# Performance work log

Measured on AMD Instinct MI355X. Metric: run time of the kernel, lower is better.

Reference implementation:

```python
import jax, jax.numpy as jnp
import numpy as np

T_V = 0.1
T_Q = 0.1
NEG_VIDEO_IOU = 0.5
POS_VIDEO_TOPK = 1
MARGIN = 0.0
EPS = 1e-12


def _normalize(x):
    # F.normalize(dim=-1) with eps clamp
    n = jnp.linalg.norm(x, axis=-1, keepdims=True)
    return x / jnp.maximum(n, EPS)


def _log_cross_entropy(pos_score, all_score, neg_mask, t, m):
    pos_exp = jnp.exp((pos_score - m) / t)
    neg_exp_sum = jnp.sum(jnp.exp(all_score / t) * neg_mask, axis=-1)
    loss = -((pos_score - m) / t - jnp.log(pos_exp + neg_exp_sum))
    return jnp.mean(loss)


def setup_inputs() -> dict:
    B, C, N, S = 32, 256, 64, 64
    key = jax.random.key(0)
    k1, k2, k3 = jax.random.split(key, 3)
    video_feats = jax.random.normal(k1, (B, C, N, N), dtype=jnp.float32)
    sents_feats = jax.random.normal(k2, (S, C), dtype=jnp.float32)
    iou2ds = jax.random.uniform(k3, (S, N, N), dtype=jnp.float32)
    mask2d = jnp.triu(jnp.ones((N, N), dtype=bool))  # P = N*(N+1)/2 = 2080
    num_targets = jnp.full((B,), S // B, dtype=jnp.int32)  # sums to S
    return {"video_feats": video_feats, "sents_feats": sents_feats,
            "num_targets": num_targets, "iou2ds": iou2ds, "mask2d": mask2d}


def reference(video_feats, sents_feats, num_targets, iou2ds, mask2d):
    B, C, N, _ = video_feats.shape
    S = sents_feats.shape[0]
    K = POS_VIDEO_TOPK
    # mask2d / num_targets are structural constants -> resolve on host
    flat_idx = np.nonzero(np.asarray(mask2d).reshape(-1))[0]   # [P]
    P = flat_idx.shape[0]
    scatter_idx = np.repeat(np.arange(B), np.asarray(num_targets))  # [S]

    # masked_select of valid proposals
    vf = video_feats.reshape(B, C, N * N)[:, :, flat_idx]      # [B,C,P]
    vf = jnp.transpose(vf, (0, 2, 1))                          # [B,P,C]
    iou = iou2ds.reshape(S, N * N)[:, flat_idx]                # [S,P]

    vf = _normalize(vf)
    sf = _normalize(sents_feats)                               # [S,C]

    # top-k proposals per sentence
    topk_idx = jax.lax.top_k(iou, K)[1]                        # [S,K]
    sv = vf[scatter_idx]                                       # [S,P,C]
    topk_video = jnp.take_along_axis(sv, topk_idx[:, :, None], axis=1)  # [S,K,C]

    # inter-video loss
    inter_video_pos = jnp.einsum('skc,sc->sk', topk_video, sf)          # [S,K]
    inter_video_all = jnp.einsum('skc,tc->skt', topk_video, sf)         # [S,K,S]
    inter_video_neg_mask = (~jnp.eye(S, dtype=bool))[:, None, :]        # [S,1,S]
    loss_inter_video = _log_cross_entropy(
        inter_video_pos, inter_video_all, inter_video_neg_mask, T_V, MARGIN)

    # inter-query loss
    inter_query_all = jnp.einsum('sc,bpc->sbp', sf, vf).reshape(S, 1, B * P)
    same_video = jnp.asarray(scatter_idx)[:, None] == jnp.arange(B)[None, :]  # [S,B]
    pos_mask = same_video[:, :, None] & (iou > NEG_VIDEO_IOU)[:, None, :]     # [S,B,P]
    inter_query_neg_mask = (~pos_mask).reshape(S, 1, B * P)
    loss_inter_query = _log_cross_entropy(
        inter_video_pos, inter_query_all, inter_query_neg_mask, T_Q, MARGIN)

    return (loss_inter_video, loss_inter_query)
```

## Files before the change

### kernel.cpp

```cpp
#include <hip/hip_runtime.h>
#include <hip/hip_bf16.h>
#include <math.h>

constexpr int B_ = 32;
constexpr int C_ = 256;
constexpr int N_ = 64;
constexpr int S_ = 64;
constexpr int NPIX = N_ * N_;
constexpr int QB = B_ * N_;

#define T_V_INV 10.0f
#define T_Q_INV 10.0f
#define NEG_IOU 0.5f

typedef __attribute__((ext_vector_type(8))) short short8;
typedef __attribute__((ext_vector_type(4))) float f32x4;

static __device__ __forceinline__ unsigned short f2bf(float x) {
  __hip_bfloat16 h = __float2bfloat16(x);
  unsigned short u;
  __builtin_memcpy(&u, &h, sizeof(u));
  return u;
}

__global__ void k_prep(const float* __restrict__ sents,
                       float* __restrict__ sf_t,
                       unsigned short* __restrict__ sf_frag) {
  int s = blockIdx.x, c = threadIdx.x;
  __shared__ float wsum[4];
  float v = sents[s * C_ + c];
  float ss = v * v;
  #pragma unroll
  for (int o = 32; o; o >>= 1) ss += __shfl_xor(ss, o);
  if ((c & 63) == 0) wsum[c >> 6] = ss;
  __syncthreads();
  float tot = wsum[0] + wsum[1] + wsum[2] + wsum[3];
  float rn = 1.0f / fmaxf(sqrtf(tot), 1e-12f);
  float o = v * rn;
  sf_t[c * S_ + s] = o;
  int ks = c >> 5, q = (c >> 3) & 3, j = c & 7;
  int mt = s >> 4, m = s & 15;
  int lane = q * 16 + m;
  sf_frag[((ks * 4 + mt) * 64 + lane) * 8 + j] = f2bf(o);
}

__global__ void k_scatter(const int* __restrict__ nt, int* __restrict__ scatter) {
  int s = threadIdx.x;
  int cum = 0, res = 0;
  for (int b = 0; b < B_; b++) {
    int nb = nt[b];
    if (s >= cum && s < cum + nb) res = b;
    cum += nb;
  }
  scatter[s] = res;
}

__global__ void k_topk(const float* __restrict__ iou, int* __restrict__ top_pix) {
  int s = blockIdx.x, tid = threadIdx.x;
  __shared__ float bval[256];
  __shared__ int bidx[256];
  float bv = -1.0f;
  int bi = 0x7fffffff;
  for (int pix = tid; pix < NPIX; pix += 256) {
    int r = pix >> 6, c0 = pix & 63;
    if (c0 >= r) {
      float v = iou[s * NPIX + pix];
      if (v > bv) { bv = v; bi = pix; }
    }
  }
  bval[tid] = bv; bidx[tid] = bi;
  __syncthreads();
  for (int st = 128; st; st >>= 1) {
    if (tid < st) {
      float ov = bval[tid + st]; int oi = bidx[tid + st];
      if (ov > bval[tid] || (ov == bval[tid] && oi < bidx[tid])) {
        bval[tid] = ov; bidx[tid] = oi;
      }
    }
    __syncthreads();
  }
  if (tid == 0) top_pix[s] = bidx[0];
}

__global__ void k_video(const float* __restrict__ V,
                        const float* __restrict__ sf_t,
                        const int* __restrict__ scatter,
                        const int* __restrict__ top_pix,
                        float* __restrict__ pos_score,
                        float* __restrict__ loss_vid) {
  int s = blockIdx.x, t = threadIdx.x;
  __shared__ float vh[C_];
  int b = scatter[s];
  int pix = top_pix[s];
  const float* vp = V + ((size_t)b * C_) * NPIX + pix;
  float vloc[4];
  float ss = 0.0f;
  #pragma unroll
  for (int k = 0; k < 4; k++) {
    vloc[k] = vp[(size_t)(t + 64 * k) * NPIX];
    ss = fmaf(vloc[k], vloc[k], ss);
  }
  #pragma unroll
  for (int o = 32; o; o >>= 1) ss += __shfl_xor(ss, o);
  float rn = 1.0f / fmaxf(sqrtf(ss), 1e-12f);
  #pragma unroll
  for (int k = 0; k < 4; k++) vh[t + 64 * k] = vloc[k] * rn;
  __syncthreads();
  float dot = 0.0f;
  #pragma unroll 8
  for (int c = 0; c < C_; c++) dot = fmaf(vh[c], sf_t[c * S_ + t], dot);
  if (t == s) pos_score[s] = dot;
  float pos = __shfl(dot, s);
  float e = (t == s) ? 0.0f : __expf(dot * T_V_INV);
  #pragma unroll
  for (int o = 32; o; o >>= 1) e += __shfl_xor(e, o);
  if (t == 0) {
    float pp = pos * T_V_INV;
    loss_vid[s] = -(pp - logf(__expf(pp) + e));
  }
}

__global__ __launch_bounds__(256) void k_query(
    const float* __restrict__ V, const float* __restrict__ iou,
    const short8* __restrict__ Afrag, const int* __restrict__ scatter,
    float* __restrict__ partials) {
  __shared__ int ssc[S_];
  __shared__ float part[4][S_];
  int tid = threadIdx.x;
  if (tid < S_) ssc[tid] = scatter[tid];
  __syncthreads();

  int b = blockIdx.x >> 6, r = blockIdx.x & 63;
  int w = tid >> 6, lane = tid & 63;
  int n = lane & 15, q = lane >> 4;
  int col = w * 16 + n;
  int pix = r * 64 + col;
  bool active = (col >= r);

  const float* vb = V + (size_t)b * C_ * NPIX + pix;
  f32x4 acc[4] = {f32x4{0,0,0,0}, f32x4{0,0,0,0}, f32x4{0,0,0,0}, f32x4{0,0,0,0}};
  float ssq = 0.0f;

  for (int ks = 0; ks < 8; ks++) {
    short8 bfrag;
    #pragma unroll
    for (int j = 0; j < 8; j++) {
      int c = ks * 32 + q * 8 + j;
      float v = active ? vb[(size_t)c * NPIX] : 0.0f;
      ssq = fmaf(v, v, ssq);
      bfrag[j] = (short)f2bf(v);
    }
    #pragma unroll
    for (int mt = 0; mt < 4; mt++) {
      short8 a = Afrag[(ks * 4 + mt) * 64 + lane];
      acc[mt] = __builtin_amdgcn_mfma_f32_16x16x32_bf16(a, bfrag, acc[mt], 0, 0, 0);
    }
  }

  ssq += __shfl_xor(ssq, 16);
  ssq += __shfl_xor(ssq, 32);
  float rs = T_Q_INV / fmaxf(sqrtf(ssq), 1e-12f);

  #pragma unroll
  for (int mt = 0; mt < 4; mt++) {
    #pragma unroll
    for (int rr = 0; rr < 4; rr++) {
      int s = mt * 16 + q * 4 + rr;
      float e = active ? __expf(acc[mt][rr] * rs) : 0.0f;
      if (active && ssc[s] == b) {
        if (iou[s * NPIX + pix] > NEG_IOU) e = 0.0f;
      }
      e += __shfl_xor(e, 1);
      e += __shfl_xor(e, 2);
      e += __shfl_xor(e, 4);
      e += __shfl_xor(e, 8);
      if (n == 0) part[w][s] = e;
    }
  }
  __syncthreads();
  if (tid < S_) {
    partials[(size_t)blockIdx.x * S_ + tid] =
        part[0][tid] + part[1][tid] + part[2][tid] + part[3][tid];
  }
}

__global__ void k_loss(const float* __restrict__ partials,
                       const float* __restrict__ pos_score,
                       float* __restrict__ loss_q) {
  int s = blockIdx.x, tid = threadIdx.x;
  __shared__ float wsum[4];
  float acc = 0.0f;
  for (int blk = tid; blk < QB; blk += 256) acc += partials[(size_t)blk * S_ + s];
  #pragma unroll
  for (int o = 32; o; o >>= 1) acc += __shfl_xor(acc, o);
  if ((tid & 63) == 0) wsum[tid >> 6] = acc;
  __syncthreads();
  if (tid == 0) {
    float neg = wsum[0] + wsum[1] + wsum[2] + wsum[3];
    float p = pos_score[s] * T_Q_INV;
    loss_q[s] = -(p - logf(__expf(p) + neg));
  }
}

__global__ void k_final(const float* __restrict__ loss_vid,
                        const float* __restrict__ loss_q,
                        float* __restrict__ out) {
  int tid = threadIdx.x;
  float lv = loss_vid[tid];
  float lq = loss_q[tid];
  #pragma unroll
  for (int o = 32; o; o >>= 1) {
    lv += __shfl_xor(lv, o);
    lq += __shfl_xor(lq, o);
  }
  if (tid == 0) {
    out[0] = lv / (float)S_;
    out[1] = lq / (float)S_;
  }
}

extern "C" void kernel_launch(void* const* d_in, const int* in_sizes, int n_in,
                              void* d_out, int out_size, void* d_ws, size_t ws_size,
                              hipStream_t stream) {
  const float* V     = (const float*)d_in[0];
  const float* sents = (const float*)d_in[1];
  const int*   nt    = (const int*)d_in[2];
  const float* iou   = (const float*)d_in[3];

  float* ws = (float*)d_ws;
  float*          sf_t    = ws;
  unsigned short* sf_frag = (unsigned short*)(ws + 16384);
  int*   scatter   = (int*)(ws + 16384 + 8192);
  int*   top_pix   = scatter + S_;
  float* pos_score = (float*)(top_pix + S_);
  float* loss_vid  = pos_score + S_;
  float* loss_q    = loss_vid + S_;
  float* partials  = loss_q + S_;

  k_prep   <<<S_, 256, 0, stream>>>(sents, sf_t, sf_frag);
  k_scatter<<<1, 64, 0, stream>>>(nt, scatter);
  k_topk   <<<S_, 256, 0, stream>>>(iou, top_pix);
  k_video  <<<S_, 64, 0, stream>>>(V, sf_t, scatter, top_pix, pos_score, loss_vid);
  k_query  <<<QB, 256, 0, stream>>>(V, iou, (const short8*)sf_frag, scatter, partials);
  k_loss   <<<S_, 256, 0, stream>>>(partials, pos_score, loss_q);
  k_final  <<<1, 64, 0, stream>>>(loss_vid, loss_q, (float*)d_out);
}
```

Baseline: 238.2 us.

## Fuse seven kernel launches into three: setup, main, and tail reduction

Merges sentence normalization, scatter computation and top-k into one setup kernel. The video-loss computation now runs as extra blocks appended to the query MFMA grid. The partial-sum reduction and final averaging are folded into a single 1024-thread tail kernel. This removes launch overhead and serialization between small kernels, but the tail reduction is now done by a single block instead of 64 blocks.

```diff
diff --git a/kernel.cpp b/kernel.cpp
--- a/kernel.cpp
+++ b/kernel.cpp
@@ -23,199 +23,198 @@
   return u;
 }
 
-__global__ void k_prep(const float* __restrict__ sents,
-                       float* __restrict__ sf_t,
-                       unsigned short* __restrict__ sf_frag) {
-  int s = blockIdx.x, c = threadIdx.x;
+__global__ __launch_bounds__(256) void k_setup(
+    const float* __restrict__ sents, const float* __restrict__ iou,
+    const int* __restrict__ nt,
+    float* __restrict__ sf_t, unsigned short* __restrict__ sf_frag,
+    int* __restrict__ scatter, int* __restrict__ top_pix) {
+  int bid = blockIdx.x, tid = threadIdx.x;
   __shared__ float wsum[4];
-  float v = sents[s * C_ + c];
-  float ss = v * v;
-  #pragma unroll
-  for (int o = 32; o; o >>= 1) ss += __shfl_xor(ss, o);
-  if ((c & 63) == 0) wsum[c >> 6] = ss;
-  __syncthreads();
-  float tot = wsum[0] + wsum[1] + wsum[2] + wsum[3];
-  float rn = 1.0f / fmaxf(sqrtf(tot), 1e-12f);
-  float o = v * rn;
-  sf_t[c * S_ + s] = o;
-  int ks = c >> 5, q = (c >> 3) & 3, j = c & 7;
-  int mt = s >> 4, m = s & 15;
-  int lane = q * 16 + m;
-  sf_frag[((ks * 4 + mt) * 64 + lane) * 8 + j] = f2bf(o);
-}
-
-__global__ void k_scatter(const int* __restrict__ nt, int* __restrict__ scatter) {
-  int s = threadIdx.x;
-  int cum = 0, res = 0;
-  for (int b = 0; b < B_; b++) {
-    int nb = nt[b];
-    if (s >= cum && s < cum + nb) res = b;
-    cum += nb;
-  }
-  scatter[s] = res;
-}
-
-__global__ void k_topk(const float* __restrict__ iou, int* __restrict__ top_pix) {
-  int s = blockIdx.x, tid = threadIdx.x;
   __shared__ float bval[256];
   __shared__ int bidx[256];
-  float bv = -1.0f;
-  int bi = 0x7fffffff;
-  for (int pix = tid; pix < NPIX; pix += 256) {
-    int r = pix >> 6, c0 = pix & 63;
-    if (c0 >= r) {
-      float v = iou[s * NPIX + pix];
-      if (v > bv) { bv = v; bi = pix; }
+
+  if (bid < S_) {
+    int s = bid, c = tid;
+    float v = sents[s * C_ + c];
+    float ss = v * v;
+    #pragma unroll
+    for (int o = 32; o; o >>= 1) ss += __shfl_xor(ss, o);
+    if ((c & 63) == 0) wsum[c >> 6] = ss;
+    __syncthreads();
+    float tot = wsum[0] + wsum[1] + wsum[2] + wsum[3];
+    float rn = 1.0f / fmaxf(sqrtf(tot), 1e-12f);
+    float o = v * rn;
+    sf_t[c * S_ + s] = o;
+    int ks = c >> 5, q = (c >> 3) & 3, j = c & 7;
+    int mt = s >> 4, m = s & 15;
+    sf_frag[((ks * 4 + mt) * 64 + (q * 16 + m)) * 8 + j] = f2bf(o);
+
+    float bv = -1.0f;
+    int bi = 0x7fffffff;
+    for (int pix = tid; pix < NPIX; pix += 256) {
+      int r = pix >> 6, c0 = pix & 63;
+      if (c0 >= r) {
+        float x = iou[s * NPIX + pix];
+        if (x > bv) { bv = x; bi = pix; }
+      }
+    }
+    bval[tid] = bv; bidx[tid] = bi;
+    __syncthreads();
+    for (int st = 128; st; st >>= 1) {
+      if (tid < st) {
+        float ov = bval[tid + st]; int oi = bidx[tid + st];
+        if (ov > bval[tid] || (ov == bval[tid] && oi < bidx[tid])) {
+          bval[tid] = ov; bidx[tid] = oi;
+        }
+      }
+      __syncthreads();
+    }
+    if (tid == 0) top_pix[s] = bidx[0];
+  } else {
+    if (tid < S_) {
+      int cum = 0, res = 0;
+      for (int b = 0; b < B_; b++) {
+        int nb = nt[b];
+        if (tid >= cum && tid < cum + nb) res = b;
+        cum += nb;
+      }
+      scatter[tid] = res;
     }
   }
-  bval[tid] = bv; bidx[tid] = bi;
-  __syncthreads();
-  for (int st = 128; st; st >>= 1) {
-    if (tid < st) {
-      float ov = bval[tid + st]; int oi = bidx[tid + st];
-      if (ov > bval[tid] || (ov == bval[tid] && oi < bidx[tid])) {
-        bval[tid] = ov; bidx[tid] = oi;
-      }
-    }
-    __syncthreads();
-  }
-  if (tid == 0) top_pix[s] = bidx[0];
-}
-
-__global__ void k_video(const float* __restrict__ V,
-                        const float* __restrict__ sf_t,
-                        const int* __restrict__ scatter,
-                        const int* __restrict__ top_pix,
-                        float* __restrict__ pos_score,
-                        float* __restrict__ loss_vid) {
-  int s = blockIdx.x, t = threadIdx.x;
-  __shared__ float vh[C_];
-  int b = scatter[s];
-  int pix = top_pix[s];
-  const float* vp = V + ((size_t)b * C_) * NPIX + pix;
-  float vloc[4];
-  float ss = 0.0f;
-  #pragma unroll
-  for (int k = 0; k < 4; k++) {
-    vloc[k] = vp[(size_t)(t + 64 * k) * NPIX];
-    ss = fmaf(vloc[k], vloc[k], ss);
-  }
-  #pragma unroll
-  for (int o = 32; o; o >>= 1) ss += __shfl_xor(ss, o);
-  float rn = 1.0f / fmaxf(sqrtf(ss), 1e-12f);
-  #pragma unroll
-  for (int k = 0; k < 4; k++) vh[t + 64 * k] = vloc[k] * rn;
-  __syncthreads();
-  float dot = 0.0f;
-  #pragma unroll 8
-  for (int c = 0; c < C_; c++) dot = fmaf(vh[c], sf_t[c * S_ + t], dot);
-  if (t == s) pos_score[s] = dot;
-  float pos = __shfl(dot, s);
-  float e = (t == s) ? 0.0f : __expf(dot * T_V_INV);
-  #pragma unroll
-  for (int o = 32; o; o >>= 1) e += __shfl_xor(e, o);
-  if (t == 0) {
-    float pp = pos * T_V_INV;
-    loss_vid[s] = -(pp - logf(__expf(pp) + e));
-  }
-}
-
-__global__ __launch_bounds__(256) void k_query(
+}
+
+__global__ __launch_bounds__(256) void k_main(
     const float* __restrict__ V, const float* __restrict__ iou,
-    const short8* __restrict__ Afrag, const int* __restrict__ scatter,
-    float* __restrict__ partials) {
+    const short8* __restrict__ Afrag, const float* __restrict__ sf_t,
+    const int* __restrict__ scatter, const int* __restrict__ top_pix,
+    float* __restrict__ partials, float* __restrict__ pos_score,
+    float* __restrict__ loss_vid) {
   __shared__ int ssc[S_];
   __shared__ float part[4][S_];
+  __shared__ float vh[C_];
+  __shared__ float red[4];
+  __shared__ float pdm[4][S_];
+
   int tid = threadIdx.x;
-  if (tid < S_) ssc[tid] = scatter[tid];
-  __syncthreads();
-
-  int b = blockIdx.x >> 6, r = blockIdx.x & 63;
-  int w = tid >> 6, lane = tid & 63;
-  int n = lane & 15, q = lane >> 4;
-  int col = w * 16 + n;
-  int pix = r * 64 + col;
-  bool active = (col >= r);
-
-  const float* vb = V + (size_t)b * C_ * NPIX + pix;
-  f32x4 acc[4] = {f32x4{0,0,0,0}, f32x4{0,0,0,0}, f32x4{0,0,0,0}, f32x4{0,0,0,0}};
-  float ssq = 0.0f;
-
-  for (int ks = 0; ks < 8; ks++) {
-    short8 bfrag;
-    #pragma unroll
-    for (int j = 0; j < 8; j++) {
-      int c = ks * 32 + q * 8 + j;
-      float v = active ? vb[(size_t)c * NPIX] : 0.0f;
-      ssq = fmaf(v, v, ssq);
-      bfrag[j] = (short)f2bf(v);
-    }
+
+  if (blockIdx.x < QB) {
+    if (tid < S_) ssc[tid] = scatter[tid];
+    __syncthreads();
+
+    int b = blockIdx.x >> 6, r = blockIdx.x & 63;
+    int w = tid >> 6, lane = tid & 63;
+    int n = lane & 15, q = lane >> 4;
+    int col = w * 16 + n;
+    int pix = r * 64 + col;
+    bool active = (col >= r);
+
+    const float* vb = V + (size_t)b * C_ * NPIX + pix;
+    f32x4 acc[4] = {f32x4{0,0,0,0}, f32x4{0,0,0,0}, f32x4{0,0,0,0}, f32x4{0,0,0,0}};
+    float ssq = 0.0f;
+
+    for (int ks = 0; ks < 8; ks++) {
+      short8 bfrag;
+      #pragma unroll
+      for (int j = 0; j < 8; j++) {
+        int c = ks * 32 + q * 8 + j;
+        float v = active ? vb[(size_t)c * NPIX] : 0.0f;
+        ssq = fmaf(v, v, ssq);
+        bfrag[j] = (short)f2bf(v);
+      }
+      #pragma unroll
+      for (int mt = 0; mt < 4; mt++) {
+        short8 a = Afrag[(ks * 4 + mt) * 64 + lane];
+        acc[mt] = __builtin_amdgcn_mfma_f32_16x16x32_bf16(a, bfrag, acc[mt], 0, 0, 0);
+      }
+    }
+
+    ssq += __shfl_xor(ssq, 16);
+    ssq += __shfl_xor(ssq, 32);
+    float rs = T_Q_INV / fmaxf(sqrtf(ssq), 1e-12f);
+
     #pragma unroll
     for (int mt = 0; mt < 4; mt++) {
-      short8 a = Afrag[(ks * 4 + mt) * 64 + lane];
-      acc[mt] = __builtin_amdgcn_mfma_f32_16x16x32_bf16(a, bfrag, acc[mt], 0, 0, 0);
+      #pragma unroll
+      for (int rr = 0; rr < 4; rr++) {
+        int s = mt * 16 + q * 4 + rr;
+        float e = active ? __expf(acc[mt][rr] * rs) : 0.0f;
+        if (active && ssc[s] == b) {
+          if (iou[s * NPIX + pix] > NEG_IOU) e = 0.0f;
+        }
+        e += __shfl_xor(e, 1);
+        e += __shfl_xor(e, 2);
+        e += __shfl_xor(e, 4);
+        e += __shfl_xor(e, 8);
+        if (n == 0) part[w][s] = e;
+      }
+    }
+    __syncthreads();
+    if (tid < S_) {
+      partials[(size_t)blockIdx.x * S_ + tid] =
+          part[0][tid] + part[1][tid] + part[2][tid] + part[3][tid];
+    }
+  } else {
+    int s = blockIdx.x - QB;
+    int b = scatter[s];
+    int pix = top_pix[s];
+    float v = V[((size_t)b * C_ + tid) * NPIX + pix];
+    float ss = v * v;
+    #pragma unroll
+    for (int o = 32; o; o >>= 1) ss += __shfl_xor(ss, o);
+    if ((tid & 63) == 0) red[tid >> 6] = ss;
+    __syncthreads();
+    float tot = red[0] + red[1] + red[2] + red[3];
+    float rn = 1.0f / fmaxf(sqrtf(tot), 1e-12f);
+    vh[tid] = v * rn;
+    __syncthreads();
+    int so = tid & 63, chunk = tid >> 6;
+    float pd = 0.0f;
+    #pragma unroll 8
+    for (int c = chunk * 64; c < chunk * 64 + 64; c++)
+      pd = fmaf(vh[c], sf_t[c * S_ + so], pd);
+    pdm[chunk][so] = pd;
+    __syncthreads();
+    if (tid < S_) {
+      float dot = pdm[0][tid] + pdm[1][tid] + pdm[2][tid] + pdm[3][tid];
+      if (tid == s) pos_score[s] = dot;
+      float pos = __shfl(dot, s);
+      float e = (tid == s) ? 0.0f : __expf(dot * T_V_INV);
+      #pragma unroll
+      for (int o = 32; o; o >>= 1) e += __shfl_xor(e, o);
+      if (tid == 0) {
+        float pp = pos * T_V_INV;
+        loss_vid[s] = -(pp - logf(__expf(pp) + e));
+      }
     }
   }
-
-  ssq += __shfl_xor(ssq, 16);
-  ssq += __shfl_xor(ssq, 32);
-  float rs = T_Q_INV / fmaxf(sqrtf(ssq), 1e-12f);
-
-  #pragma unroll
-  for (int mt = 0; mt < 4; mt++) {
-    #pragma unroll
-    for (int rr = 0; rr < 4; rr++) {
-      int s = mt * 16 + q * 4 + rr;
-      float e = active ? __expf(acc[mt][rr] * rs) : 0.0f;
-      if (active && ssc[s] == b) {
-        if (iou[s * NPIX + pix] > NEG_IOU) e = 0.0f;
-      }
-      e += __shfl_xor(e, 1);
-      e += __shfl_xor(e, 2);
-      e += __shfl_xor(e, 4);
-      e += __shfl_xor(e, 8);
-      if (n == 0) part[w][s] = e;
-    }
-  }
+}
+
+__global__ __launch_bounds__(1024) void k_tail(
+    const float* __restrict__ partials, const float* __restrict__ pos_score,
+    const float* __restrict__ loss_vid, float* __restrict__ out) {
+  int tid = threadIdx.x;
+  int s = tid & 63, g = tid >> 6;
+  __shared__ float m[16][S_];
+  float acc = 0.0f;
+  for (int blk = g; blk < QB; blk += 16) acc += partials[(size_t)blk * S_ + s];
+  m[g][s] = acc;
   __syncthreads();
   if (tid < S_) {
-    partials[(size_t)blockIdx.x * S_ + tid] =
-        part[0][tid] + part[1][tid] + part[2][tid] + part[3][tid];
-  }
-}
-
-__global__ void k_loss(const float* __restrict__ partials,
-                       const float* __restrict__ pos_score,
-                       float* __restrict__ loss_q) {
-  int s = blockIdx.x, tid = threadIdx.x;
-  __shared__ float wsum[4];
-  float acc = 0.0f;
-  for (int blk = tid; blk < QB; blk += 256) acc += partials[(size_t)blk * S_ + s];
-  #pragma unroll
-  for (int o = 32; o; o >>= 1) acc += __shfl_xor(acc, o);
-  if ((tid & 63) == 0) wsum[tid >> 6] = acc;
-  __syncthreads();
-  if (tid == 0) {
-    float neg = wsum[0] + wsum[1] + wsum[2] + wsum[3];
-    float p = pos_score[s] * T_Q_INV;
-    loss_q[s] = -(p - logf(__expf(p) + neg));
-  }
-}
-
-__global__ void k_final(const float* __restrict__ loss_vid,
-                        const float* __restrict__ loss_q,
-                        float* __restrict__ out) {
-  int tid = threadIdx.x;
-  float lv = loss_vid[tid];
-  float lq = loss_q[tid];
-  #pragma unroll
-  for (int o = 32; o; o >>= 1) {
-    lv += __shfl_xor(lv, o);
-    lq += __shfl_xor(lq, o);
-  }
-  if (tid == 0) {
-    out[0] = lv / (float)S_;
-    out[1] = lq / (float)S_;
+    float neg = 0.0f;
+    #pragma unroll
+    for (int gg = 0; gg < 16; gg++) neg += m[gg][tid];
+    float p = pos_score[tid] * T_Q_INV;
+    float lq = -(p - logf(__expf(p) + neg));
+    float lv = loss_vid[tid];
+    #pragma unroll
+    for (int o = 32; o; o >>= 1) {
+      lq += __shfl_xor(lq, o);
+      lv += __shfl_xor(lv, o);
+    }
+    if (tid == 0) {
+      out[0] = lv / (float)S_;
+      out[1] = lq / (float)S_;
+    }
   }
 }
 
@@ -234,14 +233,10 @@
   int*   top_pix   = scatter + S_;
   float* pos_score = (float*)(top_pix + S_);
   float* loss_vid  = pos_score + S_;
-  float* loss_q    = loss_vid + S_;
-  float* partials  = loss_q + S_;
-
-  k_prep   <<<S_, 256, 0, stream>>>(sents, sf_t, sf_frag);
-  k_scatter<<<1, 64, 0, stream>>>(nt, scatter);
-  k_topk   <<<S_, 256, 0, stream>>>(iou, top_pix);
-  k_video  <<<S_, 64, 0, stream>>>(V, sf_t, scatter, top_pix, pos_score, loss_vid);
-  k_query  <<<QB, 256, 0, stream>>>(V, iou, (const short8*)sf_frag, scatter, partials);
-  k_loss   <<<S_, 256, 0, stream>>>(partials, pos_score, loss_q);
-  k_final  <<<1, 64, 0, stream>>>(loss_vid, loss_q, (float*)d_out);
-}
+  float* partials  = loss_vid + S_;
+
+  k_setup<<<S_ + 1, 256, 0, stream>>>(sents, iou, nt, sf_t, sf_frag, scatter, top_pix);
+  k_main <<<QB + S_, 256, 0, stream>>>(V, iou, (const short8*)sf_frag, sf_t,
+                                       scatter, top_pix, partials, pos_score, loss_vid);
+  k_tail <<<1, 1024, 0, stream>>>(partials, pos_score, loss_vid, (float*)d_out);
+}
```

Result: slower. 249.5 us (+4.8%).
